# Performance work log

Measured on AMD Instinct MI355X. Metric: run time of the kernel, lower is better.

The kernel has to match this reference:

```python
import jax, jax.numpy as jnp
import numpy as np

D = 1024
B, T = 4, 2048


def _ln(x, g, b, eps=1e-5):
    mu = jnp.mean(x, axis=-1, keepdims=True)
    var = jnp.mean((x - mu) ** 2, axis=-1, keepdims=True)
    return (x - mu) * jax.lax.rsqrt(var + eps) * g + b


def setup_inputs() -> dict:
    key = jax.random.key(0)
    ks = jax.random.split(key, 24)
    s = 0.02
    lin = lambda k, o, i: jax.random.normal(k, (o, i), jnp.float32) * s
    return {
        "x": jax.random.normal(ks[0], (B, T, D), jnp.float32),
        "g1": jnp.ones((D,), jnp.float32),
        "be1": jnp.zeros((D,), jnp.float32),
        "w_lin1": lin(ks[1], D, D), "b_lin1": jnp.zeros((D,), jnp.float32),
        "wq": lin(ks[2], D, D), "bq": jnp.zeros((D,), jnp.float32),
        "wk": lin(ks[3], D, D), "bk": jnp.zeros((D,), jnp.float32),
        "wv": lin(ks[4], D, D), "bv": jnp.zeros((D,), jnp.float32),
        "w_lin2": lin(ks[5], D, D), "b_lin2": jnp.zeros((D,), jnp.float32),
        "g2": jnp.ones((D,), jnp.float32),
        "be2": jnp.zeros((D,), jnp.float32),
        "w_ff1": lin(ks[6], 2 * D, D), "b_ff1": jnp.zeros((2 * D,), jnp.float32),
        "w_ff2": lin(ks[7], D, 2 * D), "b_ff2": jnp.zeros((D,), jnp.float32),
    }


def reference(x, g1, be1, w_lin1, b_lin1, wq, bq, wk, bk, wv, bv,
              w_lin2, b_lin2, g2, be2, w_ff1, b_ff1, w_ff2, b_ff2):
    # x: [B,T,D]. Torch Linear: y = x @ W.T + b with W: [out,in]
    x = _ln(x, g1, be1)
    x = x @ w_lin1.T + b_lin1
    # single-head self-attention, scale = 1/sqrt(d_model) (matches source)
    q = x @ wq.T + bq
    k = x @ wk.T + bk
    v = x @ wv.T + bv
    scores = jnp.einsum('btd,bsd->bts', q, k) / jnp.sqrt(jnp.float32(x.shape[-1]))
    mask = jnp.tril(jnp.ones((x.shape[1], x.shape[1]), bool))  # [T,T]
    scores = jnp.where(mask, scores, -jnp.inf)
    probs = jax.nn.softmax(scores, axis=-1)
    attn = jnp.einsum('bts,bsd->btd', probs, v)
    x = x + (attn @ w_lin2.T + b_lin2)
    # FFN on norm2(x), exact (erf) GELU as torch default
    h = _ln(x, g2, be2)
    h = jax.nn.gelu(h @ w_ff1.T + b_ff1, approximate=False)
    x = x + (h @ w_ff2.T + b_ff2)
    return x
```

## Files before the change

### kernel.cpp

```cpp
#include <hip/hip_runtime.h>

typedef __attribute__((ext_vector_type(4))) float f32x4;
typedef __attribute__((ext_vector_type(8))) short short8;
typedef __attribute__((ext_vector_type(4))) unsigned short u16x4;
typedef __attribute__((ext_vector_type(8))) unsigned short u16x8;

#define MFMA(a, b, c) __builtin_amdgcn_mfma_f32_16x16x32_bf16(a, b, c, 0, 0, 0)
#define GLOAD16(g, l) __builtin_amdgcn_global_load_lds( \
    (const __attribute__((address_space(1))) unsigned int*)(g), \
    (__attribute__((address_space(3))) unsigned int*)(l), 16, 0, 0)
#define BARX() __builtin_amdgcn_s_barrier()
#define VM0 asm volatile("s_waitcnt vmcnt(0)" ::: "memory")

__device__ inline unsigned short f2bf(float f) {
    unsigned int u = __float_as_uint(f);
    u += 0x7fffu + ((u >> 16) & 1u);
    return (unsigned short)(u >> 16);
}

__global__ __launch_bounds__(256) void cvt_kernel(const float* __restrict__ in,
                                                  unsigned short* __restrict__ out, int n4,
                                                  float scale) {
    int i = blockIdx.x * 256 + threadIdx.x;
    if (i < n4) {
        f32x4 v = *(const f32x4*)(in + (long long)i * 4);
        u16x4 o;
#pragma unroll
        for (int j = 0; j < 4; j++) o[j] = f2bf(v[j] * scale);
        *(u16x4*)&out[(long long)i * 4] = o;
    }
}

__global__ __launch_bounds__(256) void biascat_kernel(const float* __restrict__ bq,
                                                      const float* __restrict__ bk,
                                                      float* __restrict__ out) {
    int i = blockIdx.x * 256 + threadIdx.x;
    if (i < 1024) out[i] = bq[i] * 0.03125f;
    else if (i < 2048) out[i] = bk[i - 1024];
}

__global__ __launch_bounds__(256) void ln_kernel(const float* __restrict__ x,
                                                 const float* __restrict__ g,
                                                 const float* __restrict__ be,
                                                 unsigned short* __restrict__ out) {
    const int row = blockIdx.x, tid = threadIdx.x;
    const float* px = x + (long long)row * 1024;
    f32x4 v = *(const f32x4*)(px + tid * 4);
    float s = v[0] + v[1] + v[2] + v[3];
    float q = v[0] * v[0] + v[1] * v[1] + v[2] * v[2] + v[3] * v[3];
#pragma unroll
    for (int o = 32; o; o >>= 1) { s += __shfl_xor(s, o); q += __shfl_xor(q, o); }
    __shared__ float sm[10];
    const int lane = tid & 63, wid = tid >> 6;
    if (lane == 0) { sm[wid] = s; sm[4 + wid] = q; }
    __syncthreads();
    if (tid == 0) {
        float ts = sm[0] + sm[1] + sm[2] + sm[3];
        float tq = sm[4] + sm[5] + sm[6] + sm[7];
        float mean = ts * (1.f / 1024.f);
        float var = tq * (1.f / 1024.f) - mean * mean;
        sm[8] = mean; sm[9] = rsqrtf(var + 1e-5f);
    }
    __syncthreads();
    float mean = sm[8], rs = sm[9];
    f32x4 gg = *(const f32x4*)(g + tid * 4);
    f32x4 bb = *(const f32x4*)(be + tid * 4);
    u16x4 o;
#pragma unroll
    for (int i = 0; i < 4; i++) o[i] = f2bf((v[i] - mean) * rs * gg[i] + bb[i]);
    *(u16x4*)&out[(long long)row * 1024 + tid * 4] = o;
}

__global__ __launch_bounds__(256) void softmax_kernel(float* __restrict__ S) {
    const int T = 2048;
    const int t = blockIdx.x, b = blockIdx.y, tid = threadIdx.x;
    float* row = S + ((long long)b * T + t) * T;
    const int base = tid * 8;
    f32x4 v0 = *(const f32x4*)(row + base);
    f32x4 v1 = *(const f32x4*)(row + base + 4);
    float mx = -1e30f;
#pragma unroll
    for (int i = 0; i < 4; i++) {
        if (base + i <= t)     mx = fmaxf(mx, v0[i]);
        if (base + 4 + i <= t) mx = fmaxf(mx, v1[i]);
    }
#pragma unroll
    for (int o = 32; o; o >>= 1) mx = fmaxf(mx, __shfl_xor(mx, o));
    __shared__ float sm[10];
    const int lane = tid & 63, wid = tid >> 6;
    if (lane == 0) sm[wid] = mx;
    __syncthreads();
    if (tid == 0) sm[8] = fmaxf(fmaxf(sm[0], sm[1]), fmaxf(sm[2], sm[3]));
    __syncthreads();
    float M = sm[8];
    float e[8]; float s = 0.f;
#pragma unroll
    for (int i = 0; i < 4; i++) {
        e[i]     = (base + i <= t)     ? __expf(v0[i] - M) : 0.f;
        e[4 + i] = (base + 4 + i <= t) ? __expf(v1[i] - M) : 0.f;
        s += e[i] + e[4 + i];
    }
#pragma unroll
    for (int o = 32; o; o >>= 1) s += __shfl_xor(s, o);
    if (lane == 0) sm[4 + wid] = s;
    __syncthreads();
    if (tid == 0) sm[9] = 1.f / (sm[4] + sm[5] + sm[6] + sm[7]);
    __syncthreads();
    float inv = sm[9];
    unsigned short* P = (unsigned short*)row;
    u16x8 o;
#pragma unroll
    for (int i = 0; i < 8; i++) o[i] = f2bf(e[i] * inv);
    *(u16x8*)&P[base] = o;
}

template <int MODE>
__global__ __launch_bounds__(256, 2) void gemm128(
    const unsigned short* __restrict__ A, int lda, long long sA,
    const unsigned short* __restrict__ Bw, int ldb, long long sB,
    const float* __restrict__ bias,
    const float* __restrict__ resid, long long sR,
    float* __restrict__ outf, unsigned short* __restrict__ outb,
    int ldo, long long sO, int K, float scale, int flags) {
    const int m0 = blockIdx.y * 128, n0 = blockIdx.x * 128;
    if ((flags & 1) && n0 > m0) return;
    const int bz = blockIdx.z;
    A += (long long)bz * sA; Bw += (long long)bz * sB;
    if (resid) resid += (long long)bz * sR;
    if (outf) outf += (long long)bz * sO;
    if (outb) outb += (long long)bz * sO;
    const int Keff = (flags & 2) ? (m0 + 128 < K ? m0 + 128 : K) : K;
    const int nt = Keff >> 6;

    __shared__ __align__(16) unsigned short LDS[2 * 16384];

    const int tid = threadIdx.x, lane = tid & 63, wid = tid >> 6;

    const unsigned short* srcA[4]; const unsigned short* srcB[4]; int dst[4];
#pragma unroll
    for (int l = 0; l < 4; l++) {
        int p = l * 256 + tid;
        int r = p >> 3, cs = (p & 7) ^ (r & 7);
        srcA[l] = A + (long long)(m0 + r) * lda + cs * 8;
        srcB[l] = Bw + (long long)(n0 + r) * ldb + cs * 8;
        dst[l] = l * 2048 + wid * 512;
    }

    const int wm = (wid >> 1) * 64, wn = (wid & 1) * 64;
    const int fr = lane & 15, kq = lane >> 4;
    int ao[4][2], bo[4][2];
#pragma unroll
    for (int i = 0; i < 4; i++) {
        int ra = wm + i * 16 + fr, rb = wn + i * 16 + fr;
#pragma unroll
        for (int s = 0; s < 2; s++) {
            ao[i][s] = ra * 64 + (((s * 4 + kq) ^ (ra & 7)) * 8);
            bo[i][s] = 8192 + rb * 64 + (((s * 4 + kq) ^ (rb & 7)) * 8);
        }
    }

    f32x4 acc[4][4] = {};

#pragma unroll
    for (int l = 0; l < 4; l++) GLOAD16(srcA[l], LDS + dst[l]);
#pragma unroll
    for (int l = 0; l < 4; l++) GLOAD16(srcB[l], LDS + 8192 + dst[l]);
    VM0; BARX();

    int c = 0;
    for (int t = 0; t < nt; ++t) {
        if (t + 1 < nt) {
            const int kn = (t + 1) * 64;
            unsigned short* Lp = LDS + (c ^ 1) * 16384;
#pragma unroll
            for (int l = 0; l < 4; l++) GLOAD16(srcA[l] + kn, Lp + dst[l]);
#pragma unroll
            for (int l = 0; l < 4; l++) GLOAD16(srcB[l] + kn, Lp + 8192 + dst[l]);
        }
        const unsigned short* Lc = LDS + c * 16384;
        short8 a[4], b[4];
#pragma unroll
        for (int i = 0; i < 4; i++) { a[i] = *(const short8*)&Lc[ao[i][0]];
                                      b[i] = *(const short8*)&Lc[bo[i][0]]; }
#pragma unroll
        for (int i = 0; i < 4; i++)
#pragma unroll
            for (int j = 0; j < 4; j++)
                acc[i][j] = MFMA(a[i], b[j], acc[i][j]);
#pragma unroll
        for (int i = 0; i < 4; i++) { a[i] = *(const short8*)&Lc[ao[i][1]];
                                      b[i] = *(const short8*)&Lc[bo[i][1]]; }
#pragma unroll
        for (int i = 0; i < 4; i++)
#pragma unroll
            for (int j = 0; j < 4; j++)
                acc[i][j] = MFMA(a[i], b[j], acc[i][j]);
        VM0;
        BARX();
        c ^= 1;
    }

    const int cc = lane & 15, rr = (lane >> 4) * 4;
#pragma unroll
    for (int fm = 0; fm < 4; fm++)
#pragma unroll
        for (int fn = 0; fn < 4; fn++) {
            f32x4 av = acc[fm][fn];
            int colg = n0 + wn + fn * 16 + cc;
            int rowg0 = m0 + wm + fm * 16 + rr;
            float bv = bias ? bias[colg] : 0.f;
            if (MODE == 3) {
                u16x4 o;
#pragma unroll
                for (int i = 0; i < 4; i++) o[i] = f2bf((av[i] + bv) * scale);
                *(u16x4*)&outb[(long long)colg * ldo + rowg0] = o;
            } else {
#pragma unroll
                for (int i = 0; i < 4; i++) {
                    float v = av[i] + bv;
                    long long idx = (long long)(rowg0 + i) * ldo + colg;
                    if (MODE == 0) outf[idx] = v;
                    if (MODE == 1) outf[idx] = v + resid[idx];
                    if (MODE == 2) outb[idx] = f2bf(v * scale);
                    if (MODE == 4) { outf[idx] = v; outb[idx] = f2bf(v); }
                    if (MODE == 5) outb[idx] = f2bf(0.5f * v * (1.f + erff(v * 0.70710678f)));
                }
            }
        }
}

extern "C" void kernel_launch(void* const* d_in, const int* in_sizes, int n_in,
                              void* d_out, int out_size, void* d_ws, size_t ws_size,
                              hipStream_t stream) {
    const float* x      = (const float*)d_in[0];
    const float* g1     = (const float*)d_in[1];
    const float* be1    = (const float*)d_in[2];
    const float* b_lin1 = (const float*)d_in[4];
    const float* bq     = (const float*)d_in[6];
    const float* bk     = (const float*)d_in[8];
    const float* bv     = (const float*)d_in[10];
    const float* b_lin2 = (const float*)d_in[12];
    const float* g2     = (const float*)d_in[13];
    const float* be2    = (const float*)d_in[14];
    const float* b_ff1  = (const float*)d_in[16];
    const float* b_ff2  = (const float*)d_in[18];

    const long long MB = 1024LL * 1024LL;
    char* ws = (char*)d_ws;
    unsigned short* xn1 = (unsigned short*)(ws + 0);
    unsigned short* x1b = (unsigned short*)(ws + 16 * MB);
    float*          S   = (float*)(ws + 0);
    float*          bqk = (float*)(ws + 60 * MB);
    float*          x1f = (float*)(ws + 64 * MB);
    unsigned short* xn2 = (unsigned short*)(ws + 64 * MB);
    unsigned short* qk  = (unsigned short*)(ws + 96 * MB);
    unsigned short* vT  = (unsigned short*)(ws + 128 * MB);
    unsigned short* attn= (unsigned short*)(ws + 96 * MB);
    unsigned short* h   = (unsigned short*)(ws + 96 * MB);
    float*          x2  = (float*)(ws + 144 * MB);
    unsigned short* wb1 = (unsigned short*)(ws + 176 * MB);
    unsigned short* wbq = (unsigned short*)(ws + 178 * MB);
    unsigned short* wbk = (unsigned short*)(ws + 180 * MB);
    unsigned short* wbv = (unsigned short*)(ws + 182 * MB);
    unsigned short* wb2 = (unsigned short*)(ws + 184 * MB);
    unsigned short* wbf1= (unsigned short*)(ws + 186 * MB);
    unsigned short* wbf2= (unsigned short*)(ws + 190 * MB);

    auto cvt = [&](const void* src, unsigned short* dst, long long n, float sc) {
        int n4 = (int)(n / 4);
        cvt_kernel<<<(n4 + 255) / 256, 256, 0, stream>>>((const float*)src, dst, n4, sc);
    };
    cvt(d_in[3], wb1, 1048576, 1.f);
    cvt(d_in[5], wbq, 1048576, 0.03125f);
    cvt(d_in[7], wbk, 1048576, 1.f);
    cvt(d_in[9], wbv, 1048576, 1.f);
    cvt(d_in[11], wb2, 1048576, 1.f);
    cvt(d_in[15], wbf1, 2097152, 1.f);
    cvt(d_in[17], wbf2, 2097152, 1.f);
    biascat_kernel<<<8, 256, 0, stream>>>(bq, bk, bqk);

    ln_kernel<<<8192, 256, 0, stream>>>(x, g1, be1, xn1);
    gemm128<4><<<dim3(8, 64, 1), 256, 0, stream>>>(xn1, 1024, 0, wb1, 1024, 0, b_lin1,
        nullptr, 0, x1f, x1b, 1024, 0, 1024, 1.f, 0);
    gemm128<2><<<dim3(16, 64, 1), 256, 0, stream>>>(x1b, 1024, 0, wbq, 1024, 0, bqk,
        nullptr, 0, nullptr, qk, 2048, 0, 1024, 1.f, 0);
    gemm128<3><<<dim3(8, 16, 4), 256, 0, stream>>>(x1b, 1024, 2048LL * 1024, wbv, 1024, 0, bv,
        nullptr, 0, nullptr, vT, 2048, 2097152LL, 1024, 1.f, 0);
    gemm128<0><<<dim3(16, 16, 4), 256, 0, stream>>>(qk, 2048, 4194304LL, qk + 1024, 2048, 4194304LL,
        nullptr, nullptr, 0, S, nullptr, 2048, 4194304LL, 1024, 1.f, 1);
    softmax_kernel<<<dim3(2048, 4), 256, 0, stream>>>(S);
    gemm128<2><<<dim3(8, 16, 4), 256, 0, stream>>>((unsigned short*)S, 4096, 8388608LL,
        vT, 2048, 2097152LL, nullptr, nullptr, 0, nullptr, attn, 1024, 2097152LL, 2048, 1.f, 2);
    gemm128<1><<<dim3(8, 64, 1), 256, 0, stream>>>(attn, 1024, 0, wb2, 1024, 0, b_lin2,
        x1f, 0, x2, nullptr, 1024, 0, 1024, 1.f, 0);
    ln_kernel<<<8192, 256, 0, stream>>>(x2, g2, be2, xn2);
    gemm128<5><<<dim3(16, 64, 1), 256, 0, stream>>>(xn2, 1024, 0, wbf1, 1024, 0, b_ff1,
        nullptr, 0, nullptr, h, 2048, 0, 1024, 1.f, 0);
    gemm128<1><<<dim3(8, 64, 1), 256, 0, stream>>>(h, 2048, 0, wbf2, 2048, 0, b_ff2,
        x2, 0, (float*)d_out, nullptr, 1024, 0, 2048, 1.f, 0);
}
```

Measured before the change: 483.2 us.

## Add 256x256-tile GEMM kernel for QK projection and FFN1

Adds a 512-thread GEMM with 256x256 output tiles, double-buffered LDS filled by direct global-to-LDS loads with XOR swizzle, and 8x4 MFMA fragments per wave. It is used for the two N=2048 GEMMs (fused QK projection and FFN1 with GELU). Larger tiles raise arithmetic intensity and cut global traffic per FLOP. In exchange the grid shrinks to 256 blocks and register and LDS pressure rise (128 accumulator registers per thread, 128KB LDS), which can lower occupancy.

Result: no change. 484.0 us (+0.2%).

```diff
diff --git a/kernel.cpp b/kernel.cpp
--- a/kernel.cpp
+++ b/kernel.cpp
@@ -11,6 +11,7 @@
     (__attribute__((address_space(3))) unsigned int*)(l), 16, 0, 0)
 #define BARX() __builtin_amdgcn_s_barrier()
 #define VM0 asm volatile("s_waitcnt vmcnt(0)" ::: "memory")
+#define VM8 asm volatile("s_waitcnt vmcnt(8)" ::: "memory")
 
 __device__ inline unsigned short f2bf(float f) {
     unsigned int u = __float_as_uint(f);
@@ -112,6 +113,108 @@
 #pragma unroll
     for (int i = 0; i < 8; i++) o[i] = f2bf(e[i] * inv);
     *(u16x8*)&P[base] = o;
+}
+
+template <int MODE>
+__global__ __launch_bounds__(512, 2) void gemm256(
+    const unsigned short* __restrict__ A, int lda,
+    const unsigned short* __restrict__ Bw, int ldb,
+    const float* __restrict__ bias,
+    unsigned short* __restrict__ outb, int ldo, int K, float scale) {
+    const int m0 = blockIdx.y * 256, n0 = blockIdx.x * 256;
+    const int nt = K >> 6;
+
+    __shared__ __align__(16) unsigned short LDS[2 * 32768];
+
+    const int tid = threadIdx.x, lane = tid & 63, wid = tid >> 6;
+
+    const unsigned short* srcA[4]; const unsigned short* srcB[4]; int dst[4];
+#pragma unroll
+    for (int l = 0; l < 4; l++) {
+        int p = l * 512 + tid;
+        int r = p >> 3, cs = (p & 7) ^ (r & 7);
+        srcA[l] = A + (long long)(m0 + r) * lda + cs * 8;
+        srcB[l] = Bw + (long long)(n0 + r) * ldb + cs * 8;
+        dst[l] = l * 4096 + wid * 512;
+    }
+
+    const int wm = (wid >> 2) * 128, wn = (wid & 3) * 64;
+    const int fr = lane & 15, kq = lane >> 4;
+    int ao[8][2], bo[4][2];
+#pragma unroll
+    for (int i = 0; i < 8; i++) {
+        int ra = wm + i * 16 + fr;
+#pragma unroll
+        for (int s = 0; s < 2; s++)
+            ao[i][s] = ra * 64 + (((s * 4 + kq) ^ (ra & 7)) * 8);
+    }
+#pragma unroll
+    for (int j = 0; j < 4; j++) {
+        int rb = wn + j * 16 + fr;
+#pragma unroll
+        for (int s = 0; s < 2; s++)
+            bo[j][s] = 16384 + rb * 64 + (((s * 4 + kq) ^ (rb & 7)) * 8);
+    }
+
+    f32x4 acc[8][4] = {};
+
+#pragma unroll
+    for (int l = 0; l < 4; l++) GLOAD16(srcA[l], LDS + dst[l]);
+#pragma unroll
+    for (int l = 0; l < 4; l++) GLOAD16(srcB[l], LDS + 16384 + dst[l]);
+#pragma unroll
+    for (int l = 0; l < 4; l++) GLOAD16(srcA[l] + 64, LDS + 32768 + dst[l]);
+#pragma unroll
+    for (int l = 0; l < 4; l++) GLOAD16(srcB[l] + 64, LDS + 32768 + 16384 + dst[l]);
+    VM8; BARX();
+
+    for (int t = 0; t < nt; ++t) {
+        const unsigned short* Lc = LDS + (t & 1) * 32768;
+#pragma unroll
+        for (int s = 0; s < 2; s++) {
+            short8 a[8], b[4];
+#pragma unroll
+            for (int i = 0; i < 8; i++) a[i] = *(const short8*)&Lc[ao[i][s]];
+#pragma unroll
+            for (int j = 0; j < 4; j++) b[j] = *(const short8*)&Lc[bo[j][s]];
+#pragma unroll
+            for (int i = 0; i < 8; i++)
+#pragma unroll
+                for (int j = 0; j < 4; j++)
+                    acc[i][j] = MFMA(a[i], b[j], acc[i][j]);
+        }
+        BARX();
+        if (t + 2 < nt) {
+            const int kn = (t + 2) * 64;
+            unsigned short* Lp = LDS + (t & 1) * 32768;
+#pragma unroll
+            for (int l = 0; l < 4; l++) GLOAD16(srcA[l] + kn, Lp + dst[l]);
+#pragma unroll
+            for (int l = 0; l < 4; l++) GLOAD16(srcB[l] + kn, Lp + 16384 + dst[l]);
+            VM8;
+        } else {
+            VM0;
+        }
+        BARX();
+    }
+
+    const int cc = lane & 15, rr = (lane >> 4) * 4;
+#pragma unroll
+    for (int fm = 0; fm < 8; fm++)
+#pragma unroll
+        for (int fn = 0; fn < 4; fn++) {
+            f32x4 av = acc[fm][fn];
+            int colg = n0 + wn + fn * 16 + cc;
+            int rowg0 = m0 + wm + fm * 16 + rr;
+            float bv = bias[colg];
+#pragma unroll
+            for (int i = 0; i < 4; i++) {
+                float v = av[i] + bv;
+                long long idx = (long long)(rowg0 + i) * ldo + colg;
+                if (MODE == 2) outb[idx] = f2bf(v * scale);
+                if (MODE == 5) outb[idx] = f2bf(0.5f * v * (1.f + erff(v * 0.70710678f)));
+            }
+        }
 }
 
 template <int MODE>
@@ -282,8 +385,8 @@
     ln_kernel<<<8192, 256, 0, stream>>>(x, g1, be1, xn1);
     gemm128<4><<<dim3(8, 64, 1), 256, 0, stream>>>(xn1, 1024, 0, wb1, 1024, 0, b_lin1,
         nullptr, 0, x1f, x1b, 1024, 0, 1024, 1.f, 0);
-    gemm128<2><<<dim3(16, 64, 1), 256, 0, stream>>>(x1b, 1024, 0, wbq, 1024, 0, bqk,
-        nullptr, 0, nullptr, qk, 2048, 0, 1024, 1.f, 0);
+    gemm256<2><<<dim3(8, 32, 1), 512, 0, stream>>>(x1b, 1024, wbq, 1024, bqk,
+        qk, 2048, 1024, 1.f);
     gemm128<3><<<dim3(8, 16, 4), 256, 0, stream>>>(x1b, 1024, 2048LL * 1024, wbv, 1024, 0, bv,
         nullptr, 0, nullptr, vT, 2048, 2097152LL, 1024, 1.f, 0);
     gemm128<0><<<dim3(16, 16, 4), 256, 0, stream>>>(qk, 2048, 4194304LL, qk + 1024, 2048, 4194304LL,
@@ -294,8 +397,8 @@
     gemm128<1><<<dim3(8, 64, 1), 256, 0, stream>>>(attn, 1024, 0, wb2, 1024, 0, b_lin2,
         x1f, 0, x2, nullptr, 1024, 0, 1024, 1.f, 0);
     ln_kernel<<<8192, 256, 0, stream>>>(x2, g2, be2, xn2);
-    gemm128<5><<<dim3(16, 64, 1), 256, 0, stream>>>(xn2, 1024, 0, wbf1, 1024, 0, b_ff1,
-        nullptr, 0, nullptr, h, 2048, 0, 1024, 1.f, 0);
+    gemm256<5><<<dim3(8, 32, 1), 512, 0, stream>>>(xn2, 1024, wbf1, 1024, b_ff1,
+        h, 2048, 1024, 1.f);
     gemm128<1><<<dim3(8, 64, 1), 256, 0, stream>>>(h, 2048, 0, wbf2, 2048, 0, b_ff2,
         x2, 0, (float*)d_out, nullptr, 1024, 0, 2048, 1.f, 0);
 }
```
